# Kernel optimization log

Measured on AMD Instinct MI355X. Metric: run time of the kernel, lower is better.

The kernel has to match this reference:

```python
import jax, jax.numpy as jnp
import numpy as np

N_SPECIES = 8192
N_REACTIONS = 2_097_152
NNZ_PER_REACTION = 4  # 2 reactants, 2 products
NNZ = NNZ_PER_REACTION * N_REACTIONS


def setup_inputs() -> dict:
    key = jax.random.key(0)
    ks = jax.random.split(key, 10)
    abundances = jax.random.uniform(ks[0], (N_SPECIES,), jnp.float32, 1e-12, 1e-4)
    temperature = jax.random.uniform(ks[1], (), jnp.float32, 10.0, 300.0)
    cr_rate = jax.random.uniform(ks[2], (), jnp.float32, 1e-17, 1e-15)
    fuv_rate = jax.random.uniform(ks[3], (), jnp.float32, 0.1, 10.0)
    # per-reaction modified-Arrhenius parameters
    alpha = jax.random.uniform(ks[4], (N_REACTIONS,), jnp.float32, 1e-12, 1e-9)
    beta = jax.random.uniform(ks[5], (N_REACTIONS,), jnp.float32, -1.0, 1.0)
    gamma = jax.random.uniform(ks[6], (N_REACTIONS,), jnp.float32, 0.0, 50.0)
    # reaction type: 0 = two-body Arrhenius, 1 = cosmic-ray, 2 = photodissociation
    rtype = jax.random.randint(ks[7], (N_REACTIONS,), 0, 3, dtype=jnp.int32)
    # the two reactant species of each reaction (== argwhere(incidence.T < 0))
    react_species = jax.random.randint(ks[8], (N_REACTIONS, 2), 0, N_SPECIES, dtype=jnp.int32)
    # sparse incidence matrix in COO form: rows = species, cols = reactions
    inc_rows = jax.random.randint(ks[9], (NNZ,), 0, N_SPECIES, dtype=jnp.int32)
    inc_cols = jnp.repeat(jnp.arange(N_REACTIONS, dtype=jnp.int32), NNZ_PER_REACTION)
    # first 2 entries of each reaction consumed (-1), last 2 produced (+1)
    inc_vals = jnp.where(jnp.arange(NNZ) % NNZ_PER_REACTION < 2, -1.0, 1.0).astype(jnp.float32)
    return dict(abundances=abundances, temperature=temperature, cr_rate=cr_rate,
                fuv_rate=fuv_rate, alpha=alpha, beta=beta, gamma=gamma,
                rtype=rtype, react_species=react_species,
                inc_rows=inc_rows, inc_cols=inc_cols, inc_vals=inc_vals,
                n_species=N_SPECIES)


def reference(abundances, temperature, cr_rate, fuv_rate, alpha, beta, gamma,
              rtype, react_species, inc_rows, inc_cols, inc_vals, n_species):
    # 1) batched per-reaction rate evaluation (replaces the Python loop of .at[i].set)
    T = temperature
    k_arr = alpha * (T / 300.0) ** beta * jnp.exp(-gamma / T)      # two-body
    k_cr = alpha * cr_rate                                          # cosmic-ray
    k_fuv = alpha * fuv_rate * jnp.exp(-gamma)                      # photo
    rates = jnp.where(rtype == 0, k_arr, jnp.where(rtype == 1, k_cr, k_fuv))
    # 2) multiply each rate by its reactant abundances (scatter-multiply loop fused)
    rates = rates * abundances[react_species].prod(axis=1)          # [R]
    # 3) sparse incidence @ rates -> per-species dy/dt
    contrib = inc_vals * rates[inc_cols]                            # [NNZ]
    return jax.ops.segment_sum(contrib, inc_rows, num_segments=n_species)
```

## Files before the change

### kernel.cpp

```cpp
#include <hip/hip_runtime.h>


#define NSPEC        8192
#define RPT          4
#define MAIN_BLOCKS  512
#define MAIN_THREADS 1024
#define RED_CHUNK    32
#define RED_SLICES   8

#define FIX_SCALE    0x1p73f
#define FIX_INV      0x1p-73f

__global__ __launch_bounds__(MAIN_THREADS) void jnet_fused(
    const float* __restrict__ abund,
    const float* __restrict__ temperature,
    const float* __restrict__ cr_rate,
    const float* __restrict__ fuv_rate,
    const float* __restrict__ alp,
    const float* __restrict__ bet,
    const float* __restrict__ gam,
    const int*   __restrict__ rtype,
    const int*   __restrict__ react_species,
    const int*   __restrict__ inc_rows,
    float*       __restrict__ partials,
    int n_reactions)
{
    __shared__ float    ab[NSPEC];
    __shared__ unsigned acc[NSPEC];
    const int tid = threadIdx.x;

    const uint4 z4 = {0u, 0u, 0u, 0u};
    for (int i = tid * 4; i < NSPEC; i += MAIN_THREADS * 4) {
        *(uint4*)(acc + i) = z4;
        *(float4*)(ab + i) = *(const float4*)(abund + i);
    }
    __syncthreads();

    const float T    = *temperature;
    const float crr  = *cr_rate;
    const float fuvr = *fuv_rate;
    const float LOG2E = 1.4426950408889634f;
    const float log2T300 = __log2f(T * (1.0f / 300.0f));
    const float invTln2  = LOG2E / T;

    const int base = (blockIdx.x * MAIN_THREADS + tid) * RPT;
    if (base < n_reactions) {
        const float4 a4 = *(const float4*)(alp + base);
        const float4 b4 = *(const float4*)(bet + base);
        const float4 g4 = *(const float4*)(gam + base);
        const int4   t4 = *(const int4*)(rtype + base);
        const int4  rsA = *(const int4*)(react_species + 2 * base);
        const int4  rsB = *(const int4*)(react_species + 2 * base + 4);
        const int4   q0 = *(const int4*)(inc_rows + 4 * base);
        const int4   q1 = *(const int4*)(inc_rows + 4 * base + 4);
        const int4   q2 = *(const int4*)(inc_rows + 4 * base + 8);
        const int4   q3 = *(const int4*)(inc_rows + 4 * base + 12);

        const float al[RPT] = {a4.x, a4.y, a4.z, a4.w};
        const float be[RPT] = {b4.x, b4.y, b4.z, b4.w};
        const float ga[RPT] = {g4.x, g4.y, g4.z, g4.w};
        const int   rt[RPT] = {t4.x, t4.y, t4.z, t4.w};
        const int   s0[RPT] = {rsA.x, rsA.z, rsB.x, rsB.z};
        const int   s1[RPT] = {rsA.y, rsA.w, rsB.y, rsB.w};
        const int4  qq[RPT] = {q0, q1, q2, q3};

#pragma unroll
        for (int j = 0; j < RPT; ++j) {
            const float arg = (rt[j] == 0) ? (be[j] * log2T300 - ga[j] * invTln2)
                            : ((rt[j] == 1) ? 0.0f : (-LOG2E * ga[j]));
            const float mul = (rt[j] == 0) ? 1.0f : ((rt[j] == 1) ? crr : fuvr);
            const float r = al[j] * mul * exp2f(arg) * ab[s0[j]] * ab[s1[j]];
            const int v = (int)(r * FIX_SCALE);
            const unsigned pv = (unsigned)v;
            const unsigned nv = (unsigned)(-v);
            atomicAdd(acc + qq[j].x, nv);
            atomicAdd(acc + qq[j].y, nv);
            atomicAdd(acc + qq[j].z, pv);
            atomicAdd(acc + qq[j].w, pv);
        }
    }
    __syncthreads();

    float* my = partials + (size_t)blockIdx.x * NSPEC;
    for (int i = tid * 4; i < NSPEC; i += MAIN_THREADS * 4) {
        const int4 s = *(const int4*)(acc + i);
        float4 f;
        f.x = (float)s.x * FIX_INV;
        f.y = (float)s.y * FIX_INV;
        f.z = (float)s.z * FIX_INV;
        f.w = (float)s.w * FIX_INV;
        *(float4*)(my + i) = f;
    }
}

__global__ __launch_bounds__(256) void jnet_reduce(
    const float* __restrict__ partials, float* __restrict__ out)
{
    const int by = blockIdx.x & (RED_SLICES - 1);
    const int bx = blockIdx.x >> 3;
    const int s  = by * (NSPEC / RED_SLICES) + threadIdx.x * 4;
    const float* p = partials + (size_t)bx * RED_CHUNK * NSPEC + s;

    float4 sum = {0.f, 0.f, 0.f, 0.f};
#pragma unroll 8
    for (int b = 0; b < RED_CHUNK; ++b) {
        const float4 v = *(const float4*)(p + (size_t)b * NSPEC);
        sum.x += v.x; sum.y += v.y; sum.z += v.z; sum.w += v.w;
    }
    unsafeAtomicAdd(out + s + 0, sum.x);
    unsafeAtomicAdd(out + s + 1, sum.y);
    unsafeAtomicAdd(out + s + 2, sum.z);
    unsafeAtomicAdd(out + s + 3, sum.w);
}

__global__ __launch_bounds__(256) void jnet_rhs_direct(
    const float* __restrict__ abund, const float* __restrict__ temperature,
    const float* __restrict__ cr_rate, const float* __restrict__ fuv_rate,
    const float* __restrict__ alp, const float* __restrict__ bet,
    const float* __restrict__ gam, const int* __restrict__ rtype,
    const int* __restrict__ react_species, const int* __restrict__ inc_rows,
    float* __restrict__ out, int n_reactions)
{
    const float T = *temperature, crr = *cr_rate, fuvr = *fuv_rate;
    const float LOG2E = 1.4426950408889634f;
    const float log2T300 = __log2f(T * (1.0f / 300.0f));
    const float invTln2  = LOG2E / T;
    const int base = (blockIdx.x * blockDim.x + threadIdx.x) * RPT;
    if (base >= n_reactions) return;
    const float4 a4 = *(const float4*)(alp + base);
    const float4 b4 = *(const float4*)(bet + base);
    const float4 g4 = *(const float4*)(gam + base);
    const int4   t4 = *(const int4*)(rtype + base);
    const int4  rsA = *(const int4*)(react_species + 2 * base);
    const int4  rsB = *(const int4*)(react_species + 2 * base + 4);
    const float al[RPT] = {a4.x, a4.y, a4.z, a4.w};
    const float be[RPT] = {b4.x, b4.y, b4.z, b4.w};
    const float ga[RPT] = {g4.x, g4.y, g4.z, g4.w};
    const int   rt[RPT] = {t4.x, t4.y, t4.z, t4.w};
    const int   s0[RPT] = {rsA.x, rsA.z, rsB.x, rsB.z};
    const int   s1[RPT] = {rsA.y, rsA.w, rsB.y, rsB.w};
#pragma unroll
    for (int j = 0; j < RPT; ++j) {
        const float arg = (rt[j] == 0) ? (be[j] * log2T300 - ga[j] * invTln2)
                        : ((rt[j] == 1) ? 0.0f : (-LOG2E * ga[j]));
        const float mul = (rt[j] == 0) ? 1.0f : ((rt[j] == 1) ? crr : fuvr);
        const float r = al[j] * mul * exp2f(arg) * abund[s0[j]] * abund[s1[j]];
        const int4 rows = *(const int4*)(inc_rows + 4 * (base + j));
        unsafeAtomicAdd(out + rows.x, -r);
        unsafeAtomicAdd(out + rows.y, -r);
        unsafeAtomicAdd(out + rows.z,  r);
        unsafeAtomicAdd(out + rows.w,  r);
    }
}

extern "C" void kernel_launch(void* const* d_in, const int* in_sizes, int n_in,
                              void* d_out, int out_size, void* d_ws, size_t ws_size,
                              hipStream_t stream) {
    const float* abund   = (const float*)d_in[0];
    const float* temp    = (const float*)d_in[1];
    const float* cr      = (const float*)d_in[2];
    const float* fuv     = (const float*)d_in[3];
    const float* alp     = (const float*)d_in[4];
    const float* bet     = (const float*)d_in[5];
    const float* gam     = (const float*)d_in[6];
    const int*   rtype   = (const int*)d_in[7];
    const int*   rspec   = (const int*)d_in[8];
    const int*   incrows = (const int*)d_in[9];
    float* out = (float*)d_out;
    const int R = in_sizes[4];

    hipMemsetAsync(d_out, 0, (size_t)out_size * sizeof(float), stream);

    const size_t partials_bytes = (size_t)MAIN_BLOCKS * NSPEC * sizeof(float);
    if (ws_size >= partials_bytes) {
        float* partials = (float*)d_ws;
        hipLaunchKernelGGL(jnet_fused, dim3(MAIN_BLOCKS), dim3(MAIN_THREADS),
                           0, stream, abund, temp, cr, fuv, alp, bet, gam,
                           rtype, rspec, incrows, partials, R);
        hipLaunchKernelGGL(jnet_reduce,
                           dim3((MAIN_BLOCKS / RED_CHUNK) * RED_SLICES), dim3(256),
                           0, stream, partials, out);
    } else {
        const int threads = 256;
        const int blocks  = (R + threads * RPT - 1) / (threads * RPT);
        hipLaunchKernelGGL(jnet_rhs_direct, dim3(blocks), dim3(threads), 0, stream,
                           abund, temp, cr, fuv, alp, bet, gam, rtype, rspec,
                           incrows, out, R);
    }
}
```

Measured before the change: 177.4 us.

## Halve main blocks with 8 reactions per thread and single-pass direct-store reduction

The main kernel now processes 8 reactions per thread across 256 blocks instead of 4 across 512, halving the per-block shared-memory zeroing and the partial-histogram writes. The reduction kernel sums all 256 partials per species in one pass and stores the result directly, which removes the output memset and the global float atomics. The cost is fewer, longer-running blocks in the main kernel and a reduction launched with only 8 blocks, each walking a long serial loop.

```diff
diff --git a/kernel.cpp b/kernel.cpp
--- a/kernel.cpp
+++ b/kernel.cpp
@@ -2,11 +2,9 @@
 
 
 #define NSPEC        8192
-#define RPT          4
-#define MAIN_BLOCKS  512
+#define RPT          8
+#define MAIN_BLOCKS  256
 #define MAIN_THREADS 1024
-#define RED_CHUNK    32
-#define RED_SLICES   8
 
 #define FIX_SCALE    0x1p73f
 #define FIX_INV      0x1p-73f
@@ -45,38 +43,42 @@
 
     const int base = (blockIdx.x * MAIN_THREADS + tid) * RPT;
     if (base < n_reactions) {
-        const float4 a4 = *(const float4*)(alp + base);
-        const float4 b4 = *(const float4*)(bet + base);
-        const float4 g4 = *(const float4*)(gam + base);
-        const int4   t4 = *(const int4*)(rtype + base);
-        const int4  rsA = *(const int4*)(react_species + 2 * base);
-        const int4  rsB = *(const int4*)(react_species + 2 * base + 4);
-        const int4   q0 = *(const int4*)(inc_rows + 4 * base);
-        const int4   q1 = *(const int4*)(inc_rows + 4 * base + 4);
-        const int4   q2 = *(const int4*)(inc_rows + 4 * base + 8);
-        const int4   q3 = *(const int4*)(inc_rows + 4 * base + 12);
+#pragma unroll
+        for (int h = 0; h < 2; ++h) {
+            const int b4i = base + h * 4;
+            const float4 a4 = *(const float4*)(alp + b4i);
+            const float4 bb = *(const float4*)(bet + b4i);
+            const float4 g4 = *(const float4*)(gam + b4i);
+            const int4   t4 = *(const int4*)(rtype + b4i);
+            const int4  rsA = *(const int4*)(react_species + 2 * b4i);
+            const int4  rsB = *(const int4*)(react_species + 2 * b4i + 4);
+            const int4   q0 = *(const int4*)(inc_rows + 4 * b4i);
+            const int4   q1 = *(const int4*)(inc_rows + 4 * b4i + 4);
+            const int4   q2 = *(const int4*)(inc_rows + 4 * b4i + 8);
+            const int4   q3 = *(const int4*)(inc_rows + 4 * b4i + 12);
 
-        const float al[RPT] = {a4.x, a4.y, a4.z, a4.w};
-        const float be[RPT] = {b4.x, b4.y, b4.z, b4.w};
-        const float ga[RPT] = {g4.x, g4.y, g4.z, g4.w};
-        const int   rt[RPT] = {t4.x, t4.y, t4.z, t4.w};
-        const int   s0[RPT] = {rsA.x, rsA.z, rsB.x, rsB.z};
-        const int   s1[RPT] = {rsA.y, rsA.w, rsB.y, rsB.w};
-        const int4  qq[RPT] = {q0, q1, q2, q3};
+            const float al[4] = {a4.x, a4.y, a4.z, a4.w};
+            const float be[4] = {bb.x, bb.y, bb.z, bb.w};
+            const float ga[4] = {g4.x, g4.y, g4.z, g4.w};
+            const int   rt[4] = {t4.x, t4.y, t4.z, t4.w};
+            const int   s0[4] = {rsA.x, rsA.z, rsB.x, rsB.z};
+            const int   s1[4] = {rsA.y, rsA.w, rsB.y, rsB.w};
+            const int4  qq[4] = {q0, q1, q2, q3};
 
 #pragma unroll
-        for (int j = 0; j < RPT; ++j) {
-            const float arg = (rt[j] == 0) ? (be[j] * log2T300 - ga[j] * invTln2)
-                            : ((rt[j] == 1) ? 0.0f : (-LOG2E * ga[j]));
-            const float mul = (rt[j] == 0) ? 1.0f : ((rt[j] == 1) ? crr : fuvr);
-            const float r = al[j] * mul * exp2f(arg) * ab[s0[j]] * ab[s1[j]];
-            const int v = (int)(r * FIX_SCALE);
-            const unsigned pv = (unsigned)v;
-            const unsigned nv = (unsigned)(-v);
-            atomicAdd(acc + qq[j].x, nv);
-            atomicAdd(acc + qq[j].y, nv);
-            atomicAdd(acc + qq[j].z, pv);
-            atomicAdd(acc + qq[j].w, pv);
+            for (int j = 0; j < 4; ++j) {
+                const float arg = (rt[j] == 0) ? (be[j] * log2T300 - ga[j] * invTln2)
+                                : ((rt[j] == 1) ? 0.0f : (-LOG2E * ga[j]));
+                const float mul = (rt[j] == 0) ? 1.0f : ((rt[j] == 1) ? crr : fuvr);
+                const float r = al[j] * mul * exp2f(arg) * ab[s0[j]] * ab[s1[j]];
+                const int v = (int)(r * FIX_SCALE);
+                const unsigned pv = (unsigned)v;
+                const unsigned nv = (unsigned)(-v);
+                atomicAdd(acc + qq[j].x, nv);
+                atomicAdd(acc + qq[j].y, nv);
+                atomicAdd(acc + qq[j].z, pv);
+                atomicAdd(acc + qq[j].w, pv);
+            }
         }
     }
     __syncthreads();
@@ -96,21 +98,16 @@
 __global__ __launch_bounds__(256) void jnet_reduce(
     const float* __restrict__ partials, float* __restrict__ out)
 {
-    const int by = blockIdx.x & (RED_SLICES - 1);
-    const int bx = blockIdx.x >> 3;
-    const int s  = by * (NSPEC / RED_SLICES) + threadIdx.x * 4;
-    const float* p = partials + (size_t)bx * RED_CHUNK * NSPEC + s;
+    const int s = (blockIdx.x * 256 + threadIdx.x) * 4;
+    const float* p = partials + s;
 
     float4 sum = {0.f, 0.f, 0.f, 0.f};
 #pragma unroll 8
-    for (int b = 0; b < RED_CHUNK; ++b) {
+    for (int b = 0; b < MAIN_BLOCKS; ++b) {
         const float4 v = *(const float4*)(p + (size_t)b * NSPEC);
         sum.x += v.x; sum.y += v.y; sum.z += v.z; sum.w += v.w;
     }
-    unsafeAtomicAdd(out + s + 0, sum.x);
-    unsafeAtomicAdd(out + s + 1, sum.y);
-    unsafeAtomicAdd(out + s + 2, sum.z);
-    unsafeAtomicAdd(out + s + 3, sum.w);
+    *(float4*)(out + s) = sum;
 }
 
 __global__ __launch_bounds__(256) void jnet_rhs_direct(
@@ -125,7 +122,7 @@
     const float LOG2E = 1.4426950408889634f;
     const float log2T300 = __log2f(T * (1.0f / 300.0f));
     const float invTln2  = LOG2E / T;
-    const int base = (blockIdx.x * blockDim.x + threadIdx.x) * RPT;
+    const int base = (blockIdx.x * blockDim.x + threadIdx.x) * 4;
     if (base >= n_reactions) return;
     const float4 a4 = *(const float4*)(alp + base);
     const float4 b4 = *(const float4*)(bet + base);
@@ -133,14 +130,14 @@
     const int4   t4 = *(const int4*)(rtype + base);
     const int4  rsA = *(const int4*)(react_species + 2 * base);
     const int4  rsB = *(const int4*)(react_species + 2 * base + 4);
-    const float al[RPT] = {a4.x, a4.y, a4.z, a4.w};
-    const float be[RPT] = {b4.x, b4.y, b4.z, b4.w};
-    const float ga[RPT] = {g4.x, g4.y, g4.z, g4.w};
-    const int   rt[RPT] = {t4.x, t4.y, t4.z, t4.w};
-    const int   s0[RPT] = {rsA.x, rsA.z, rsB.x, rsB.z};
-    const int   s1[RPT] = {rsA.y, rsA.w, rsB.y, rsB.w};
+    const float al[4] = {a4.x, a4.y, a4.z, a4.w};
+    const float be[4] = {b4.x, b4.y, b4.z, b4.w};
+    const float ga[4] = {g4.x, g4.y, g4.z, g4.w};
+    const int   rt[4] = {t4.x, t4.y, t4.z, t4.w};
+    const int   s0[4] = {rsA.x, rsA.z, rsB.x, rsB.z};
+    const int   s1[4] = {rsA.y, rsA.w, rsB.y, rsB.w};
 #pragma unroll
-    for (int j = 0; j < RPT; ++j) {
+    for (int j = 0; j < 4; ++j) {
         const float arg = (rt[j] == 0) ? (be[j] * log2T300 - ga[j] * invTln2)
                         : ((rt[j] == 1) ? 0.0f : (-LOG2E * ga[j]));
         const float mul = (rt[j] == 0) ? 1.0f : ((rt[j] == 1) ? crr : fuvr);
@@ -169,20 +166,18 @@
     float* out = (float*)d_out;
     const int R = in_sizes[4];
 
-    hipMemsetAsync(d_out, 0, (size_t)out_size * sizeof(float), stream);
-
     const size_t partials_bytes = (size_t)MAIN_BLOCKS * NSPEC * sizeof(float);
     if (ws_size >= partials_bytes) {
         float* partials = (float*)d_ws;
         hipLaunchKernelGGL(jnet_fused, dim3(MAIN_BLOCKS), dim3(MAIN_THREADS),
                            0, stream, abund, temp, cr, fuv, alp, bet, gam,
                            rtype, rspec, incrows, partials, R);
-        hipLaunchKernelGGL(jnet_reduce,
-                           dim3((MAIN_BLOCKS / RED_CHUNK) * RED_SLICES), dim3(256),
+        hipLaunchKernelGGL(jnet_reduce, dim3(NSPEC / (256 * 4)), dim3(256),
                            0, stream, partials, out);
     } else {
+        hipMemsetAsync(d_out, 0, (size_t)out_size * sizeof(float), stream);
         const int threads = 256;
-        const int blocks  = (R + threads * RPT - 1) / (threads * RPT);
+        const int blocks  = (R + threads * 4 - 1) / (threads * 4);
         hipLaunchKernelGGL(jnet_rhs_direct, dim3(blocks), dim3(threads), 0, stream,
                            abund, temp, cr, fuv, alp, bet, gam, rtype, rspec,
                            incrows, out, R);
```

New measurement: 187.9 us. 5.9% more time.
